# Performance work log

Hardware: AMD Instinct MI355X
Metric: run time of the kernel (lower is better)

## Reference

```python
import jax, jax.numpy as jnp
import numpy as np

KP_EXTENT = 1.2  # influence radius of each kernel point (init arg KP_extent)
SHADOW_COORD = 1e6  # shadow point coordinate for padding (as in original KPConv)


def setup_inputs() -> dict:
    key = jax.random.key(0)
    k1, k2, k3, k4, k5, k6 = jax.random.split(key, 6)
    N, Ns, H, K, Cin, Cout = 20000, 20000, 40, 15, 128, 128
    q_pts = jax.random.uniform(k1, (N, 3), dtype=jnp.float32)
    s_pts = jax.random.uniform(k2, (Ns, 3), dtype=jnp.float32)
    neighb_inds = jax.random.randint(k3, (N, H), 0, Ns, dtype=jnp.int32)
    x = jax.random.normal(k4, (Ns, Cin), dtype=jnp.float32)
    # kernel point positions inside the sphere (stand-in for load_kernels output)
    kernel_points = jax.random.normal(k5, (K, 3), dtype=jnp.float32) * 0.5
    kernel_points = kernel_points.at[0].set(0.0)  # fixed='center'
    weights = jax.random.normal(k6, (K, Cin, Cout), dtype=jnp.float32) * (1.0 / np.sqrt(Cin))
    return {"q_pts": q_pts, "s_pts": s_pts, "neighb_inds": neighb_inds,
            "x": x, "kernel_points": kernel_points, "weights": weights}


def reference(q_pts, s_pts, neighb_inds, x, kernel_points, weights):
    # Pad support points with a far-away shadow point and features with a zero row,
    # so out-of-range neighbor index Ns contributes nothing (original KPConv trick).
    s_pad = jnp.concatenate([s_pts, jnp.full((1, s_pts.shape[1]), SHADOW_COORD, s_pts.dtype)], axis=0)
    x_pad = jnp.concatenate([x, jnp.zeros((1, x.shape[1]), x.dtype)], axis=0)

    # Gather neighbor coords, center on query points: [N, H, 3]
    neighbors = s_pad[neighb_inds] - q_pts[:, None, :]

    # Squared distance to every kernel point: [N, H, K]
    diff = neighbors[:, :, None, :] - kernel_points[None, None, :, :]
    sq_dist = jnp.sum(diff * diff, axis=-1)

    # Linear influence weights, aggregation_mode='sum': [N, K, H]
    all_weights = jnp.clip(1.0 - jnp.sqrt(sq_dist) / KP_EXTENT, 0.0, None)
    all_weights = jnp.swapaxes(all_weights, 1, 2)

    # Gather neighbor features: [N, H, Cin]
    neighb_x = x_pad[neighb_inds]

    # Influence-weighted aggregation over neighbors: [N, K, Cin]
    weighted = jnp.einsum('nkh,nhc->nkc', all_weights, neighb_x)

    # Per-kernel-point linear maps, summed over kernel points: [N, Cout]
    out = jnp.einsum('nkc,kcd->nd', weighted, weights)
    return out
```

## Files before the change

kernel.cpp:

```cpp
#include <hip/hip_runtime.h>

#define KP   15
#define HN   40
#define CIN  128
#define COUT 128
#define KDIM (KP*CIN)
#define KP_EXT_INV (1.0f/1.2f)

typedef __bf16 bf16x8 __attribute__((ext_vector_type(8)));
typedef __bf16 bf16x4 __attribute__((ext_vector_type(4)));
typedef float  f32x4  __attribute__((ext_vector_type(4)));

__device__ inline void async_copy16(const void* g, void* lds) {
    __builtin_amdgcn_global_load_lds(
        (const __attribute__((address_space(1))) unsigned int*)g,
        (__attribute__((address_space(3))) unsigned int*)lds, 16, 0, 0);
}
#define LGKM0() __asm__ __volatile__("s_waitcnt lgkmcnt(0)" ::: "memory")

__global__ __launch_bounds__(256)
void kpconv_prep(const float* __restrict__ x, const float* __restrict__ W,
                 __bf16* __restrict__ xb, __bf16* __restrict__ Wt,
                 int nx_elems, int nxB)
{
    __shared__ float sW[32][133];
    const int b = blockIdx.x;
    const int t = threadIdx.x;

    if (b < nxB) {
        const int e0 = (b*256 + t) * 8;
        if (e0 + 8 <= nx_elems) {
            const float4 f0 = *(const float4*)(x + e0);
            const float4 f1 = *(const float4*)(x + e0 + 4);
            bf16x8 v;
            v[0]=(__bf16)f0.x; v[1]=(__bf16)f0.y; v[2]=(__bf16)f0.z; v[3]=(__bf16)f0.w;
            v[4]=(__bf16)f1.x; v[5]=(__bf16)f1.y; v[6]=(__bf16)f1.z; v[7]=(__bf16)f1.w;
            *(bf16x8*)(xb + e0) = v;
        } else {
            for (int e = e0; e < nx_elems; ++e) xb[e] = (__bf16)x[e];
        }
    } else {
        const int kc0 = (b - nxB) * 32;
        #pragma unroll
        for (int i = 0; i < 4; ++i) {
            const int off = t*4 + i*1024;
            const int r = off >> 7, c = off & 127;
            const float4 f = *(const float4*)(W + (size_t)(kc0 + r)*COUT + c);
            sW[r][c+0]=f.x; sW[r][c+1]=f.y; sW[r][c+2]=f.z; sW[r][c+3]=f.w;
        }
        __syncthreads();
        #pragma unroll
        for (int i = 0; i < 2; ++i) {
            const int id = t + i*256;
            const int d  = id >> 2, ch = id & 3;
            bf16x8 v;
            #pragma unroll
            for (int j = 0; j < 8; ++j) v[j] = (__bf16)sW[ch*8 + j][d];
            *(bf16x8*)(Wt + (size_t)d*KDIM + kc0 + ch*8) = v;
        }
    }
}

__global__ __launch_bounds__(256, 3)
void kpconv_aggregate(const float* __restrict__ q_pts,
                      const float* __restrict__ s_pts,
                      const int*   __restrict__ nb,
                      const __bf16* __restrict__ xb,
                      const float* __restrict__ kpts,
                      __bf16* __restrict__ wsA,
                      int N, int Ns)
{
    __shared__ __align__(16) __bf16 sXt[4][4][128][8];
    __shared__ __align__(16) float4 s_nd[4][2][HN];
    __shared__ int                  s_idx[4][2][HN];

    const int t  = threadIdx.x;
    const int wv = t >> 6;
    const int l  = t & 63;
    const int m  = l & 15;
    const int q  = l >> 4;
    const int nbase = (blockIdx.x*4 + wv)*2;

    #pragma unroll
    for (int pp = 0; pp < 2; ++pp) {
        if (l < HN) {
            const int n = nbase + pp;
            int idx = nb[n*HN + l];
            float dx, dy, dz;
            if (idx >= 0 && idx < Ns) {
                dx = s_pts[idx*3+0] - q_pts[n*3+0];
                dy = s_pts[idx*3+1] - q_pts[n*3+1];
                dz = s_pts[idx*3+2] - q_pts[n*3+2];
            } else { idx = 0; dx = dy = dz = 2.0e6f; }
            s_idx[wv][pp][l] = idx;
            s_nd[wv][pp][l]  = make_float4(dx, dy, dz, dx*dx + dy*dy + dz*dz);
        }
    }
    LGKM0();

    uint4 g[2][5][2];
    #pragma unroll
    for (int pp = 0; pp < 2; ++pp) {
        #pragma unroll
        for (int it = 0; it < 5; ++it) {
            const int h0 = (it < 4) ? (it*8 + 2*q) : (32 + 2*q);
            g[pp][it][0] = *(const uint4*)(xb + (size_t)s_idx[wv][pp][h0  ]*CIN + m*8);
            g[pp][it][1] = *(const uint4*)(xb + (size_t)s_idx[wv][pp][h0+1]*CIN + m*8);
        }
    }

    float kx=0.f, ky=0.f, kz=0.f;
    if (m < KP) { kx = kpts[m*3+0]; ky = kpts[m*3+1]; kz = kpts[m*3+2]; }
    const float kk  = kx*kx + ky*ky + kz*kz;
    const float kx2 = -2.f*kx, ky2 = -2.f*ky, kz2 = -2.f*kz;

    bf16x8 wfrag[2][2];
    #pragma unroll
    for (int pp = 0; pp < 2; ++pp) {
        #pragma unroll
        for (int ks = 0; ks < 2; ++ks) {
            #pragma unroll
            for (int j = 0; j < 8; ++j) {
                const int h = ks*32 + q*8 + j;
                float w = 0.f;
                if (m < KP && h < HN) {
                    const float4 nd = s_nd[wv][pp][h];
                    const float d2 = fmaf(nd.x, kx2,
                                     fmaf(nd.y, ky2,
                                     fmaf(nd.z, kz2, nd.w + kk)));
                    const float d = __builtin_amdgcn_sqrtf(d2);
                    w = fmaxf(fmaf(d, -KP_EXT_INV, 1.0f), 0.f);
                }
                wfrag[pp][ks][j] = (__bf16)w;
            }
        }
    }

    #pragma unroll
    for (int pp = 0; pp < 2; ++pp) {
        const int n = nbase + pp;
        f32x4 acc[8];
        #pragma unroll
        for (int nt = 0; nt < 8; ++nt) acc[nt] = (f32x4){0.f,0.f,0.f,0.f};

        #pragma unroll
        for (int ks = 0; ks < 2; ++ks) {
            const int itBeg = ks ? 4 : 0;
            const int itEnd = ks ? 5 : 4;
            #pragma unroll
            for (int it = itBeg; it < itEnd; ++it) {
                const unsigned av[4] = {g[pp][it][0].x, g[pp][it][0].y,
                                        g[pp][it][0].z, g[pp][it][0].w};
                const unsigned bv[4] = {g[pp][it][1].x, g[pp][it][1].y,
                                        g[pp][it][1].z, g[pp][it][1].w};
                const int hc = ks ? 0 : it;
                const int dw = q;
                unsigned* plane = (unsigned*)&sXt[wv][hc][0][0];
                #pragma unroll
                for (int j = 0; j < 8; ++j) {
                    const unsigned v = __builtin_amdgcn_perm(
                        bv[j>>1], av[j>>1], (j&1) ? 0x07060302u : 0x05040100u);
                    const int p = m*8 + (j ^ (m & 7));
                    plane[p*4 + dw] = v;
                }
            }
            LGKM0();

            #pragma unroll
            for (int nt = 0; nt < 8; ++nt) {
                const int cc = nt*16 + m;
                const int p  = (cc & ~7) | ((cc & 7) ^ ((cc >> 3) & 7));
                bf16x8 xf = *(const bf16x8*)&sXt[wv][q][p][0];
                acc[nt] = __builtin_amdgcn_mfma_f32_16x16x32_bf16(
                              xf, wfrag[pp][ks], acc[nt], 0, 0, 0);
            }
        }

        if (m < KP) {
            #pragma unroll
            for (int nt = 0; nt < 8; ++nt) {
                bf16x4 v;
                #pragma unroll
                for (int r = 0; r < 4; ++r) v[r] = (__bf16)acc[nt][r];
                *(bf16x4*)(wsA + (size_t)n*KDIM + m*CIN + nt*16 + q*4) = v;
            }
        }
    }
}

#define GBM 32

__global__ __launch_bounds__(256, 4)
void kpconv_gemm(const __bf16* __restrict__ A,
                 const __bf16* __restrict__ Bt,
                 float* __restrict__ out, int M)
{
    __shared__ __align__(16) __bf16 sA[GBM*128];

    const int t     = threadIdx.x;
    const int wv    = t >> 6;
    const int l     = t & 63;
    const int mlane = l & 15;
    const int q     = l >> 4;
    const int m0    = blockIdx.x * GBM;

    const int r0  = t >> 4;
    const int pos = t & 15;

    const __bf16* Brow0 = Bt + (size_t)(wv*32 + mlane) * KDIM;
    const __bf16* Brow1 = Brow0 + (size_t)16 * KDIM;

    f32x4 acc[2][2];
    #pragma unroll
    for (int i = 0; i < 2; ++i)
        #pragma unroll
        for (int j = 0; j < 2; ++j) acc[i][j] = (f32x4){0.f,0.f,0.f,0.f};

    for (int k0 = 0; k0 < KDIM; k0 += 128) {
        #pragma unroll
        for (int p = 0; p < 2; ++p) {
            const int row = r0 + p*16;
            const int ch  = pos ^ (row & 15);
            async_copy16(A + (size_t)(m0 + row)*KDIM + k0 + ch*8,
                         (char*)sA + (p*256 + t)*16);
        }
        __syncthreads();

        bf16x8 bfr[2][4];
        #pragma unroll
        for (int ks = 0; ks < 4; ++ks) {
            bfr[0][ks] = *(const bf16x8*)(Brow0 + k0 + ks*32 + q*8);
            bfr[1][ks] = *(const bf16x8*)(Brow1 + k0 + ks*32 + q*8);
        }

        #pragma unroll
        for (int ks = 0; ks < 4; ++ks) {
            bf16x8 af[2];
            #pragma unroll
            for (int mt = 0; mt < 2; ++mt) {
                const int row = mt*16 + mlane;
                const int p   = (ks*4 + q) ^ (row & 15);
                af[mt] = *(const bf16x8*)&sA[row*128 + p*8];
            }
            #pragma unroll
            for (int mt = 0; mt < 2; ++mt)
                #pragma unroll
                for (int j = 0; j < 2; ++j)
                    acc[mt][j] = __builtin_amdgcn_mfma_f32_16x16x32_bf16(
                                     af[mt], bfr[j][ks], acc[mt][j], 0, 0, 0);
        }
        __syncthreads();
    }

    #pragma unroll
    for (int mt = 0; mt < 2; ++mt)
        #pragma unroll
        for (int j = 0; j < 2; ++j)
            #pragma unroll
            for (int r = 0; r < 4; ++r)
                out[(size_t)(m0 + mt*16 + q*4 + r)*COUT + wv*32 + j*16 + mlane]
                    = acc[mt][j][r];
}

#define TM 8
#define WSTR (KP*CIN + 4)

__global__ __launch_bounds__(256, 2)
void kpconv_fused(const float* __restrict__ q_pts,
                  const float* __restrict__ s_pts,
                  const int*   __restrict__ nb,
                  const float* __restrict__ x,
                  const float* __restrict__ kpts,
                  const float* __restrict__ W,
                  float* __restrict__ out,
                  int N, int Ns)
{
    __shared__ float s_kp[KP*3];
    __shared__ float s_nd2[HN*3];
    __shared__ int   s_idx2[HN];
    __shared__ float s_w[KP][HN];
    __shared__ float s_wt[TM*WSTR];

    const int t  = threadIdx.x;
    const int n0 = (int)blockIdx.x * TM;
    if (t < KP*3) s_kp[t] = kpts[t];
    const int c = t & (CIN-1);
    const int g = t >> 7;

    for (int mm = 0; mm < TM; ++mm) {
        const int n = n0 + mm;
        if (t < HN) {
            float dx = 1e6f, dy = 1e6f, dz = 1e6f;
            int idx = 0;
            if (n < N) {
                idx = nb[n*HN + t];
                if (idx >= 0 && idx < Ns) {
                    dx = s_pts[idx*3+0] - q_pts[n*3+0];
                    dy = s_pts[idx*3+1] - q_pts[n*3+1];
                    dz = s_pts[idx*3+2] - q_pts[n*3+2];
                } else idx = 0;
            }
            s_idx2[t] = idx;
            s_nd2[t*3+0] = dx; s_nd2[t*3+1] = dy; s_nd2[t*3+2] = dz;
        }
        __syncthreads();
        for (int task = t; task < KP*HN; task += 256) {
            const int k = task / HN;
            const int h = task - k*HN;
            const float dx = s_nd2[h*3+0] - s_kp[k*3+0];
            const float dy = s_nd2[h*3+1] - s_kp[k*3+1];
            const float dz = s_nd2[h*3+2] - s_kp[k*3+2];
            s_w[k][h] = fmaxf(1.0f - sqrtf(dx*dx+dy*dy+dz*dz)*KP_EXT_INV, 0.0f);
        }
        __syncthreads();
        float facc[8];
        #pragma unroll
        for (int j = 0; j < 8; ++j) facc[j] = 0.0f;
        #pragma unroll 8
        for (int h = 0; h < HN; ++h) {
            const float xv = x[s_idx2[h]*CIN + c];
            #pragma unroll
            for (int j = 0; j < 8; ++j) {
                const int k = g + 2*j;
                if (k < KP) facc[j] += s_w[k][h] * xv;
            }
        }
        #pragma unroll
        for (int j = 0; j < 8; ++j) {
            const int k = g + 2*j;
            if (k < KP) s_wt[mm*WSTR + k*CIN + c] = facc[j];
        }
        __syncthreads();
    }

    const int m3 = t >> 5;
    const int d0 = (t & 31) * 4;
    const float* wm = &s_wt[m3*WSTR];
    float ax = 0.f, ay = 0.f, az = 0.f, aw = 0.f;
    #pragma unroll 4
    for (int kc = 0; kc < KP*CIN; ++kc) {
        const float  wvv = wm[kc];
        const float4 wr = *(const float4*)&W[kc*COUT + d0];
        ax += wvv * wr.x; ay += wvv * wr.y; az += wvv * wr.z; aw += wvv * wr.w;
    }
    const int n = n0 + m3;
    if (n < N) {
        float4 o; o.x = ax; o.y = ay; o.z = az; o.w = aw;
        *(float4*)&out[n*COUT + d0] = o;
    }
}

extern "C" void kernel_launch(void* const* d_in, const int* in_sizes, int n_in,
                              void* d_out, int out_size, void* d_ws, size_t ws_size,
                              hipStream_t stream) {
    const float* q_pts = (const float*)d_in[0];
    const float* s_pts = (const float*)d_in[1];
    const int*   nb    = (const int*)  d_in[2];
    const float* x     = (const float*)d_in[3];
    const float* kpts  = (const float*)d_in[4];
    const float* W     = (const float*)d_in[5];
    float* out = (float*)d_out;

    const int N  = in_sizes[0] / 3;
    const int Ns = in_sizes[1] / 3;
    const int nx = in_sizes[3];

    const size_t needA = (size_t)N * KDIM * sizeof(__bf16);
    const size_t needB = (size_t)COUT * KDIM * sizeof(__bf16);
    const size_t needX = (size_t)nx * sizeof(__bf16);

    if (ws_size >= needA + needB + needX && (N % 8) == 0 && (N % GBM) == 0
        && (KDIM % 128) == 0) {
        __bf16* wsA = (__bf16*)d_ws;
        __bf16* wsB = (__bf16*)((char*)d_ws + needA);
        __bf16* wsX = (__bf16*)((char*)d_ws + needA + needB);

        const int nxB = (nx/8 + 255) / 256;
        const int nwB = KDIM / 32;
        hipLaunchKernelGGL(kpconv_prep, dim3(nxB + nwB), dim3(256), 0, stream,
                           x, W, wsX, wsB, nx, nxB);
        hipLaunchKernelGGL(kpconv_aggregate, dim3(N/8), dim3(256), 0, stream,
                           q_pts, s_pts, nb, wsX, kpts, wsA, N, Ns);
        hipLaunchKernelGGL(kpconv_gemm, dim3(N/GBM), dim3(256), 0, stream,
                           wsA, wsB, out, N);
    } else {
        const int grid = (N + TM - 1) / TM;
        hipLaunchKernelGGL(kpconv_fused, dim3(grid), dim3(256), 0, stream,
                           q_pts, s_pts, nb, x, kpts, W, out, N, Ns);
    }
}
```

Measured before the change: 164.9 us.

## Use one-wave aggregate blocks and split-K GEMM with LDS-staged B and atomics

The aggregate kernel now launches one 64-thread block per query point instead of four waves handling two points each. This shrinks LDS and register use per block, at the cost of more blocks to schedule. The GEMM is split into two K halves along grid.y, and B tiles are staged into LDS through async copies instead of being loaded directly from global memory. Results are combined with float atomicAdd after a memset of the output, which doubles GEMM parallelism but adds atomic traffic and an extra memset launch.

```diff
diff --git a/kernel.cpp b/kernel.cpp
--- a/kernel.cpp
+++ b/kernel.cpp
@@ -61,7 +61,7 @@
     }
 }
 
-__global__ __launch_bounds__(256, 3)
+__global__ __launch_bounds__(64, 4)
 void kpconv_aggregate(const float* __restrict__ q_pts,
                       const float* __restrict__ s_pts,
                       const int*   __restrict__ nb,
@@ -70,43 +70,34 @@
                       __bf16* __restrict__ wsA,
                       int N, int Ns)
 {
-    __shared__ __align__(16) __bf16 sXt[4][4][128][8];
-    __shared__ __align__(16) float4 s_nd[4][2][HN];
-    __shared__ int                  s_idx[4][2][HN];
-
-    const int t  = threadIdx.x;
-    const int wv = t >> 6;
-    const int l  = t & 63;
-    const int m  = l & 15;
-    const int q  = l >> 4;
-    const int nbase = (blockIdx.x*4 + wv)*2;
-
-    #pragma unroll
-    for (int pp = 0; pp < 2; ++pp) {
-        if (l < HN) {
-            const int n = nbase + pp;
-            int idx = nb[n*HN + l];
-            float dx, dy, dz;
-            if (idx >= 0 && idx < Ns) {
-                dx = s_pts[idx*3+0] - q_pts[n*3+0];
-                dy = s_pts[idx*3+1] - q_pts[n*3+1];
-                dz = s_pts[idx*3+2] - q_pts[n*3+2];
-            } else { idx = 0; dx = dy = dz = 2.0e6f; }
-            s_idx[wv][pp][l] = idx;
-            s_nd[wv][pp][l]  = make_float4(dx, dy, dz, dx*dx + dy*dy + dz*dz);
-        }
+    __shared__ __align__(16) __bf16 sXt[4][128][8];
+    __shared__ __align__(16) float4 s_nd[HN];
+    __shared__ int                  s_idx[HN];
+
+    const int l = threadIdx.x;
+    const int m = l & 15;
+    const int q = l >> 4;
+    const int n = blockIdx.x;
+
+    if (l < HN) {
+        int idx = nb[n*HN + l];
+        float dx, dy, dz;
+        if (idx >= 0 && idx < Ns) {
+            dx = s_pts[idx*3+0] - q_pts[n*3+0];
+            dy = s_pts[idx*3+1] - q_pts[n*3+1];
+            dz = s_pts[idx*3+2] - q_pts[n*3+2];
+        } else { idx = 0; dx = dy = dz = 2.0e6f; }
+        s_idx[l] = idx;
+        s_nd[l]  = make_float4(dx, dy, dz, dx*dx + dy*dy + dz*dz);
     }
     LGKM0();
 
-    uint4 g[2][5][2];
-    #pragma unroll
-    for (int pp = 0; pp < 2; ++pp) {
-        #pragma unroll
-        for (int it = 0; it < 5; ++it) {
-            const int h0 = (it < 4) ? (it*8 + 2*q) : (32 + 2*q);
-            g[pp][it][0] = *(const uint4*)(xb + (size_t)s_idx[wv][pp][h0  ]*CIN + m*8);
-            g[pp][it][1] = *(const uint4*)(xb + (size_t)s_idx[wv][pp][h0+1]*CIN + m*8);
-        }
+    uint4 g[5][2];
+    #pragma unroll
+    for (int it = 0; it < 5; ++it) {
+        const int h0 = (it < 4) ? (it*8 + 2*q) : (32 + 2*q);
+        g[it][0] = *(const uint4*)(xb + (size_t)s_idx[h0  ]*CIN + m*8);
+        g[it][1] = *(const uint4*)(xb + (size_t)s_idx[h0+1]*CIN + m*8);
     }
 
     float kx=0.f, ky=0.f, kz=0.f;
@@ -114,88 +105,80 @@
     const float kk  = kx*kx + ky*ky + kz*kz;
     const float kx2 = -2.f*kx, ky2 = -2.f*ky, kz2 = -2.f*kz;
 
-    bf16x8 wfrag[2][2];
-    #pragma unroll
-    for (int pp = 0; pp < 2; ++pp) {
-        #pragma unroll
-        for (int ks = 0; ks < 2; ++ks) {
+    bf16x8 wfrag[2];
+    #pragma unroll
+    for (int ks = 0; ks < 2; ++ks) {
+        #pragma unroll
+        for (int j = 0; j < 8; ++j) {
+            const int h = ks*32 + q*8 + j;
+            float w = 0.f;
+            if (m < KP && h < HN) {
+                const float4 nd = s_nd[h];
+                const float d2 = fmaf(nd.x, kx2,
+                                 fmaf(nd.y, ky2,
+                                 fmaf(nd.z, kz2, nd.w + kk)));
+                const float d = __builtin_amdgcn_sqrtf(d2);
+                w = fmaxf(fmaf(d, -KP_EXT_INV, 1.0f), 0.f);
+            }
+            wfrag[ks][j] = (__bf16)w;
+        }
+    }
+
+    f32x4 acc[8];
+    #pragma unroll
+    for (int nt = 0; nt < 8; ++nt) acc[nt] = (f32x4){0.f,0.f,0.f,0.f};
+
+    #pragma unroll
+    for (int ks = 0; ks < 2; ++ks) {
+        const int itBeg = ks ? 4 : 0;
+        const int itEnd = ks ? 5 : 4;
+        #pragma unroll
+        for (int it = itBeg; it < itEnd; ++it) {
+            const unsigned av[4] = {g[it][0].x, g[it][0].y, g[it][0].z, g[it][0].w};
+            const unsigned bv[4] = {g[it][1].x, g[it][1].y, g[it][1].z, g[it][1].w};
+            const int hc = ks ? 0 : it;
+            unsigned* plane = (unsigned*)&sXt[hc][0][0];
             #pragma unroll
             for (int j = 0; j < 8; ++j) {
-                const int h = ks*32 + q*8 + j;
-                float w = 0.f;
-                if (m < KP && h < HN) {
-                    const float4 nd = s_nd[wv][pp][h];
-                    const float d2 = fmaf(nd.x, kx2,
-                                     fmaf(nd.y, ky2,
-                                     fmaf(nd.z, kz2, nd.w + kk)));
-                    const float d = __builtin_amdgcn_sqrtf(d2);
-                    w = fmaxf(fmaf(d, -KP_EXT_INV, 1.0f), 0.f);
-                }
-                wfrag[pp][ks][j] = (__bf16)w;
-            }
-        }
-    }
-
-    #pragma unroll
-    for (int pp = 0; pp < 2; ++pp) {
-        const int n = nbase + pp;
-        f32x4 acc[8];
-        #pragma unroll
-        for (int nt = 0; nt < 8; ++nt) acc[nt] = (f32x4){0.f,0.f,0.f,0.f};
-
-        #pragma unroll
-        for (int ks = 0; ks < 2; ++ks) {
-            const int itBeg = ks ? 4 : 0;
-            const int itEnd = ks ? 5 : 4;
-            #pragma unroll
-            for (int it = itBeg; it < itEnd; ++it) {
-                const unsigned av[4] = {g[pp][it][0].x, g[pp][it][0].y,
-                                        g[pp][it][0].z, g[pp][it][0].w};
-                const unsigned bv[4] = {g[pp][it][1].x, g[pp][it][1].y,
-                                        g[pp][it][1].z, g[pp][it][1].w};
-                const int hc = ks ? 0 : it;
-                const int dw = q;
-                unsigned* plane = (unsigned*)&sXt[wv][hc][0][0];
-                #pragma unroll
-                for (int j = 0; j < 8; ++j) {
-                    const unsigned v = __builtin_amdgcn_perm(
-                        bv[j>>1], av[j>>1], (j&1) ? 0x07060302u : 0x05040100u);
-                    const int p = m*8 + (j ^ (m & 7));
-                    plane[p*4 + dw] = v;
-                }
-            }
-            LGKM0();
-
-            #pragma unroll
-            for (int nt = 0; nt < 8; ++nt) {
-                const int cc = nt*16 + m;
-                const int p  = (cc & ~7) | ((cc & 7) ^ ((cc >> 3) & 7));
-                bf16x8 xf = *(const bf16x8*)&sXt[wv][q][p][0];
-                acc[nt] = __builtin_amdgcn_mfma_f32_16x16x32_bf16(
-                              xf, wfrag[pp][ks], acc[nt], 0, 0, 0);
-            }
-        }
-
-        if (m < KP) {
-            #pragma unroll
-            for (int nt = 0; nt < 8; ++nt) {
-                bf16x4 v;
-                #pragma unroll
-                for (int r = 0; r < 4; ++r) v[r] = (__bf16)acc[nt][r];
-                *(bf16x4*)(wsA + (size_t)n*KDIM + m*CIN + nt*16 + q*4) = v;
-            }
+                const unsigned v = __builtin_amdgcn_perm(
+                    bv[j>>1], av[j>>1], (j&1) ? 0x07060302u : 0x05040100u);
+                const int p = m*8 + (j ^ (m & 7));
+                plane[p*4 + q] = v;
+            }
+        }
+        LGKM0();
+
+        #pragma unroll
+        for (int nt = 0; nt < 8; ++nt) {
+            const int cc = nt*16 + m;
+            const int p  = (cc & ~7) | ((cc & 7) ^ ((cc >> 3) & 7));
+            bf16x8 xf = *(const bf16x8*)&sXt[q][p][0];
+            acc[nt] = __builtin_amdgcn_mfma_f32_16x16x32_bf16(
+                          xf, wfrag[ks], acc[nt], 0, 0, 0);
+        }
+    }
+
+    if (m < KP) {
+        #pragma unroll
+        for (int nt = 0; nt < 8; ++nt) {
+            bf16x4 v;
+            #pragma unroll
+            for (int r = 0; r < 4; ++r) v[r] = (__bf16)acc[nt][r];
+            *(bf16x4*)(wsA + (size_t)n*KDIM + m*CIN + nt*16 + q*4) = v;
         }
     }
 }
 
 #define GBM 32
+#define GBK 128
 
 __global__ __launch_bounds__(256, 4)
 void kpconv_gemm(const __bf16* __restrict__ A,
                  const __bf16* __restrict__ Bt,
                  float* __restrict__ out, int M)
 {
-    __shared__ __align__(16) __bf16 sA[GBM*128];
+    __shared__ __align__(16) __bf16 sA[GBM*GBK];
+    __shared__ __align__(16) __bf16 sB[COUT*GBK];
 
     const int t     = threadIdx.x;
     const int wv    = t >> 6;
@@ -204,11 +187,11 @@
     const int q     = l >> 4;
     const int m0    = blockIdx.x * GBM;
 
-    const int r0  = t >> 4;
-    const int pos = t & 15;
-
-    const __bf16* Brow0 = Bt + (size_t)(wv*32 + mlane) * KDIM;
-    const __bf16* Brow1 = Brow0 + (size_t)16 * KDIM;
+    const int itBeg = blockIdx.y ? 8 : 0;
+    const int itEnd = blockIdx.y ? 15 : 8;
+
+    const int rA = t >> 4;
+    const int pA = t & 15;
 
     f32x4 acc[2][2];
     #pragma unroll
@@ -216,38 +199,45 @@
         #pragma unroll
         for (int j = 0; j < 2; ++j) acc[i][j] = (f32x4){0.f,0.f,0.f,0.f};
 
-    for (int k0 = 0; k0 < KDIM; k0 += 128) {
-        #pragma unroll
-        for (int p = 0; p < 2; ++p) {
-            const int row = r0 + p*16;
-            const int ch  = pos ^ (row & 15);
-            async_copy16(A + (size_t)(m0 + row)*KDIM + k0 + ch*8,
-                         (char*)sA + (p*256 + t)*16);
-        }
-        __syncthreads();
-
-        bf16x8 bfr[2][4];
+    for (int it = itBeg; it < itEnd; ++it) {
+        const int k0 = it * GBK;
+        #pragma unroll
+        for (int pass = 0; pass < 2; ++pass) {
+            const int r  = rA + pass*16;
+            const int ch = pA ^ (r & 15);
+            async_copy16(A + (size_t)(m0 + r)*KDIM + k0 + ch*8,
+                         (char*)sA + pass*4096 + wv*1024 + l*16);
+        }
+        #pragma unroll
+        for (int pass = 0; pass < 8; ++pass) {
+            const int r  = rA + pass*16;
+            const int ch = pA ^ (r & 15);
+            async_copy16(Bt + (size_t)r*KDIM + k0 + ch*8,
+                         (char*)sB + pass*4096 + wv*1024 + l*16);
+        }
+        __syncthreads();
+
         #pragma unroll
         for (int ks = 0; ks < 4; ++ks) {
-            bfr[0][ks] = *(const bf16x8*)(Brow0 + k0 + ks*32 + q*8);
-            bfr[1][ks] = *(const bf16x8*)(Brow1 + k0 + ks*32 + q*8);
-        }
-
-        #pragma unroll
-        for (int ks = 0; ks < 4; ++ks) {
-            bf16x8 af[2];
+            bf16x8 af[2], bfr[2];
             #pragma unroll
             for (int mt = 0; mt < 2; ++mt) {
                 const int row = mt*16 + mlane;
                 const int p   = (ks*4 + q) ^ (row & 15);
-                af[mt] = *(const bf16x8*)&sA[row*128 + p*8];
+                af[mt] = *(const bf16x8*)&sA[row*GBK + p*8];
+            }
+            #pragma unroll
+            for (int j = 0; j < 2; ++j) {
+                const int row = (wv*2 + j)*16 + mlane;
+                const int p   = (ks*4 + q) ^ (row & 15);
+                bfr[j] = *(const bf16x8*)&sB[row*GBK + p*8];
             }
             #pragma unroll
             for (int mt = 0; mt < 2; ++mt)
                 #pragma unroll
                 for (int j = 0; j < 2; ++j)
                     acc[mt][j] = __builtin_amdgcn_mfma_f32_16x16x32_bf16(
-                                     af[mt], bfr[j][ks], acc[mt][j], 0, 0, 0);
+                                     af[mt], bfr[j], acc[mt][j], 0, 0, 0);
         }
         __syncthreads();
     }
@@ -258,8 +248,8 @@
         for (int j = 0; j < 2; ++j)
             #pragma unroll
             for (int r = 0; r < 4; ++r)
-                out[(size_t)(m0 + mt*16 + q*4 + r)*COUT + wv*32 + j*16 + mlane]
-                    = acc[mt][j][r];
+                atomicAdd(&out[(size_t)(m0 + mt*16 + q*4 + r)*COUT
+                               + (wv*2+j)*16 + mlane], acc[mt][j][r]);
 }
 
 #define TM 8
@@ -369,19 +359,19 @@
     const size_t needB = (size_t)COUT * KDIM * sizeof(__bf16);
     const size_t needX = (size_t)nx * sizeof(__bf16);
 
-    if (ws_size >= needA + needB + needX && (N % 8) == 0 && (N % GBM) == 0
-        && (KDIM % 128) == 0) {
+    if (ws_size >= needA + needB + needX && (N % GBM) == 0 && (KDIM % 128) == 0) {
         __bf16* wsA = (__bf16*)d_ws;
         __bf16* wsB = (__bf16*)((char*)d_ws + needA);
         __bf16* wsX = (__bf16*)((char*)d_ws + needA + needB);
 
         const int nxB = (nx/8 + 255) / 256;
         const int nwB = KDIM / 32;
+        hipMemsetAsync(out, 0, (size_t)out_size * sizeof(float), stream);
         hipLaunchKernelGGL(kpconv_prep, dim3(nxB + nwB), dim3(256), 0, stream,
                            x, W, wsX, wsB, nx, nxB);
-        hipLaunchKernelGGL(kpconv_aggregate, dim3(N/8), dim3(256), 0, stream,
+        hipLaunchKernelGGL(kpconv_aggregate, dim3(N), dim3(64), 0, stream,
                            q_pts, s_pts, nb, wsX, kpts, wsA, N, Ns);
-        hipLaunchKernelGGL(kpconv_gemm, dim3(N/GBM), dim3(256), 0, stream,
+        hipLaunchKernelGGL(kpconv_gemm, dim3(N/GBM, 2), dim3(256), 0, stream,
                            wsA, wsB, out, N);
     } else {
         const int grid = (N + TM - 1) / TM;
```

Result: faster. 144.1 us (-12.6%).
